# Kernel tuning notes

Measured on AMD Instinct MI355X. Metric: run time of the kernel, lower is better.

Reference implementation:

```python
import jax, jax.numpy as jnp
import numpy as np

B, C, H, W = 8, 128, 256, 256
N_POS, N_NEG = 2048, 8192
TEMPERATURE = 1.0
EPS = 1e-6


def setup_inputs() -> dict:
    key = jax.random.key(0)
    k0, k1, k2, k3, k4, k5, k6 = jax.random.split(key, 7)
    predict_seg_map = jax.random.normal(k0, (B, C, H, W), dtype=jnp.float32)
    # Random pixel-location samples (stand-in for nonzero+randperm sampling,
    # which the original detaches -> constants w.r.t. the loss).
    pos_b = jax.random.randint(k1, (N_POS,), 0, B, dtype=jnp.int32)
    pos_h = jax.random.randint(k2, (N_POS,), 0, H, dtype=jnp.int32)
    pos_w = jax.random.randint(k3, (N_POS,), 0, W, dtype=jnp.int32)
    neg_b = jax.random.randint(k4, (N_NEG,), 0, B, dtype=jnp.int32)
    neg_h = jax.random.randint(k5, (N_NEG,), 0, H, dtype=jnp.int32)
    neg_w = jax.random.randint(k6, (N_NEG,), 0, W, dtype=jnp.int32)
    return {
        "predict_seg_map": predict_seg_map,
        "pos_b": pos_b, "pos_h": pos_h, "pos_w": pos_w,
        "neg_b": neg_b, "neg_h": neg_h, "neg_w": neg_w,
    }


def _l2_normalize(x):
    # Matches nn.CosineSimilarity(dim=-1, eps=1e-6): clamp norm from below.
    n = jnp.sqrt(jnp.sum(x * x, axis=-1, keepdims=True))
    return x / jnp.maximum(n, EPS)


def reference(predict_seg_map, pos_b, pos_h, pos_w, neg_b, neg_h, neg_w):
    # Irregular gather of pixel embeddings: [N, C]
    pos_logits = predict_seg_map[pos_b, :, pos_h, pos_w]
    neg_logits = predict_seg_map[neg_b, :, neg_h, neg_w]

    pos_n = _l2_normalize(pos_logits)  # [N_POS, C]
    neg_n = _l2_normalize(neg_logits)  # [N_NEG, C]

    # Cosine similarity matrices via GEMM on unit vectors.
    pos_sim = jnp.einsum('ic,jc->ij', pos_n, pos_n)  # [N_POS, N_POS]
    neg_sim = jnp.einsum('ic,jc->ij', pos_n, neg_n)  # [N_POS, N_NEG]

    exp_pos = jnp.exp(pos_sim / TEMPERATURE)
    # Original subtracts exp(1.0) (diagonal self-similarity at T=1).
    pos_row_sum = jnp.sum(exp_pos, axis=1) - jnp.exp(jnp.float32(1.0))
    neg_row_sum = jnp.sum(jnp.exp(neg_sim / TEMPERATURE), axis=1)

    likelihood = pos_row_sum / (pos_row_sum + neg_row_sum)
    nll = -jnp.mean(jnp.log(likelihood))
    return nll
```

## Files before the change

kernel.cpp:

```cpp
#include <hip/hip_runtime.h>
#include <hip/hip_bf16.h>
#include <math.h>

#define BB      8
#define C_CH    128
#define HH      256
#define WW      256
#define N_POS   2048
#define N_NEG   8192
#define N_ROWS  (N_POS + N_NEG)
#define EPS_N   1e-6f

#define NI2     (N_POS / 64)
#define NJS     (N_ROWS / 64)
#define NJSLAB      (N_ROWS / 64)
#define NJSLAB_POS  (N_POS / 64)

#define PANEL   512

typedef __attribute__((ext_vector_type(8))) short bf16x8;
typedef __attribute__((ext_vector_type(4))) float f32x4;


__global__ __launch_bounds__(256) void gather_norm_kernel(
    const float* __restrict__ seg,
    const int* __restrict__ pb, const int* __restrict__ ph, const int* __restrict__ pw,
    const int* __restrict__ nb, const int* __restrict__ nh, const int* __restrict__ nw,
    ushort* __restrict__ hi_t, ushort* __restrict__ lo_t)
{
    const int wave = threadIdx.x >> 6;
    const int lane = threadIdx.x & 63;
    const int row  = blockIdx.x * 4 + wave;
    if (row >= N_ROWS) return;

    int b, h, w;
    if (row < N_POS) { b = pb[row]; h = ph[row]; w = pw[row]; }
    else { const int r = row - N_POS; b = nb[r]; h = nh[r]; w = nw[r]; }

    const size_t cs   = (size_t)HH * WW;
    const size_t base = (size_t)b * C_CH * cs + (size_t)h * WW + (size_t)w;

    const float v0 = seg[base + (size_t)lane * cs];
    const float v1 = seg[base + (size_t)(lane + 64) * cs];

    float ss = v0 * v0 + v1 * v1;
#pragma unroll
    for (int m = 1; m < 64; m <<= 1) ss += __shfl_xor(ss, m, 64);

    const float n  = fmaxf(sqrtf(ss), EPS_N);
    const float u0 = v0 / n;
    const float u1 = v1 / n;

    const __hip_bfloat16 h0 = __float2bfloat16(u0);
    const __hip_bfloat16 h1 = __float2bfloat16(u1);
    const __hip_bfloat16 l0 = __float2bfloat16(u0 - __bfloat162float(h0));
    const __hip_bfloat16 l1 = __float2bfloat16(u1 - __bfloat162float(h1));

    const int tile = row >> 4;
    const int lr   = row & 15;

    const int e0 = lane;
    const int ks0 = e0 >> 5, lk0 = (e0 & 31) >> 3, ke0 = e0 & 7;
    const size_t o0 = ((size_t)(tile * 4 + ks0) * 64 + lk0 * 16 + lr) * 8 + ke0;

    const int e1 = lane + 64;
    const int ks1 = e1 >> 5, lk1 = (e1 & 31) >> 3, ke1 = e1 & 7;
    const size_t o1 = ((size_t)(tile * 4 + ks1) * 64 + lk1 * 16 + lr) * 8 + ke1;

    hi_t[o0] = __hip_bfloat16_raw(h0).x;  lo_t[o0] = __hip_bfloat16_raw(l0).x;
    hi_t[o1] = __hip_bfloat16_raw(h1).x;  lo_t[o1] = __hip_bfloat16_raw(l1).x;
}

__global__ __launch_bounds__(64) void sim_mfma_kernel(
    const ushort* __restrict__ hi_t, const ushort* __restrict__ lo_t,
    float* __restrict__ partial)
{
    const int bid = blockIdx.x;
    const int it  = bid / NJS;
    const int js  = bid % NJS;
    const int lane = threadIdx.x & 63;

    const int iw0 = it * 64;

    const int lr = lane & 15;
    const int lk = lane >> 4;

    f32x4 acc[4][4];
#pragma unroll
    for (int m = 0; m < 4; ++m)
#pragma unroll
        for (int n = 0; n < 4; ++n) acc[m][n] = (f32x4){0.f, 0.f, 0.f, 0.f};

#pragma unroll
    for (int ks = 0; ks < 4; ++ks) {
        bf16x8 ah[4], al[4], bh[4], bl[4];
#pragma unroll
        for (int m = 0; m < 4; ++m) {
            const size_t pa = ((size_t)((it * 4 + m) * 4 + ks)) * PANEL + lane * 8;
            ah[m] = *(const bf16x8*)&hi_t[pa];
            al[m] = *(const bf16x8*)&lo_t[pa];
        }
#pragma unroll
        for (int n = 0; n < 4; ++n) {
            const size_t pb2 = ((size_t)((js * 4 + n) * 4 + ks)) * PANEL + lane * 8;
            bh[n] = *(const bf16x8*)&hi_t[pb2];
            bl[n] = *(const bf16x8*)&lo_t[pb2];
        }

#pragma unroll
        for (int n = 0; n < 4; ++n) {
#pragma unroll
            for (int m = 0; m < 4; ++m) {
                acc[m][n] = __builtin_amdgcn_mfma_f32_16x16x32_bf16(ah[m], bh[n], acc[m][n], 0, 0, 0);
                acc[m][n] = __builtin_amdgcn_mfma_f32_16x16x32_bf16(ah[m], bl[n], acc[m][n], 0, 0, 0);
                acc[m][n] = __builtin_amdgcn_mfma_f32_16x16x32_bf16(al[m], bh[n], acc[m][n], 0, 0, 0);
            }
        }
    }

#pragma unroll
    for (int m = 0; m < 4; ++m) {
        float s0 = 0.f, s1 = 0.f, s2 = 0.f, s3 = 0.f;
#pragma unroll
        for (int n = 0; n < 4; ++n) {
            s0 += expf(acc[m][n][0]);
            s1 += expf(acc[m][n][1]);
            s2 += expf(acc[m][n][2]);
            s3 += expf(acc[m][n][3]);
        }
        float s[4] = {s0, s1, s2, s3};
#pragma unroll
        for (int r = 0; r < 4; ++r) {
            float v = s[r];
            v += __shfl_xor(v, 1, 64);
            v += __shfl_xor(v, 2, 64);
            v += __shfl_xor(v, 4, 64);
            v += __shfl_xor(v, 8, 64);
            if (lr == 0) {
                const int row = iw0 + m * 16 + lk * 4 + r;
                partial[(size_t)js * N_POS + row] = v;
            }
        }
    }
}

__global__ __launch_bounds__(256) void rowred_kernel(
    const float* __restrict__ partial, float* __restrict__ bsum)
{
    const int t   = threadIdx.x;
    const int row = blockIdx.x * 256 + t;

    float P = 0.f;
#pragma unroll
    for (int s = 0; s < NJSLAB_POS; ++s) P += partial[(size_t)s * N_POS + row];

    float a0 = 0.f, a1 = 0.f, a2 = 0.f, a3 = 0.f;
    for (int s0 = NJSLAB_POS; s0 < NJSLAB; s0 += 16) {
        float v[16];
#pragma unroll
        for (int i = 0; i < 16; ++i)
            v[i] = partial[(size_t)(s0 + i) * N_POS + row];
#pragma unroll
        for (int i = 0; i < 16; i += 4) {
            a0 += v[i]; a1 += v[i + 1]; a2 += v[i + 2]; a3 += v[i + 3];
        }
    }
    const float Nv = (a0 + a1) + (a2 + a3);

    const float p = P - 2.71828182845904523536f;
    const float term = logf(p) - logf(p + Nv);

    __shared__ float red[256];
    red[t] = term;
    __syncthreads();
    for (int s = 128; s > 0; s >>= 1) {
        if (t < s) red[t] += red[t + s];
        __syncthreads();
    }
    if (t == 0) bsum[blockIdx.x] = red[0];
}

__global__ __launch_bounds__(64) void final_kernel(
    const float* __restrict__ bsum, float* __restrict__ out)
{
    if (threadIdx.x == 0) {
        float s = 0.f;
#pragma unroll
        for (int i = 0; i < N_POS / 256; ++i) s += bsum[i];
        out[0] = -s / (float)N_POS;
    }
}

extern "C" void kernel_launch(void* const* d_in, const int* in_sizes, int n_in,
                              void* d_out, int out_size, void* d_ws, size_t ws_size,
                              hipStream_t stream)
{
    const float* seg = (const float*)d_in[0];
    const int* pb = (const int*)d_in[1];
    const int* ph = (const int*)d_in[2];
    const int* pw = (const int*)d_in[3];
    const int* nb = (const int*)d_in[4];
    const int* nh = (const int*)d_in[5];
    const int* nw = (const int*)d_in[6];
    float* out = (float*)d_out;

    ushort* hi_t = (ushort*)d_ws;
    ushort* lo_t = hi_t + (size_t)N_ROWS * C_CH;
    float* partial = (float*)(lo_t + (size_t)N_ROWS * C_CH);
    float* bsum    = partial + (size_t)NJSLAB * N_POS;

    gather_norm_kernel<<<dim3((N_ROWS + 3) / 4), dim3(256), 0, stream>>>(
        seg, pb, ph, pw, nb, nh, nw, hi_t, lo_t);

    sim_mfma_kernel<<<dim3(NI2 * NJS), dim3(64), 0, stream>>>(hi_t, lo_t, partial);

    rowred_kernel<<<dim3(N_POS / 256), dim3(256), 0, stream>>>(partial, bsum);
    final_kernel<<<dim3(1), dim3(64), 0, stream>>>(bsum, out);
}
```

Measured before the change: 66.70 us.

## Share B slab across four waves via LDS in similarity MFMA kernel

Each block of the similarity kernel now runs four waves covering 256 query rows against one 64-row key slab. The key slab's hi/lo bf16 panels are staged once into shared memory and read by all four waves, instead of each single-wave block reloading them from global memory. This is meant to cut redundant global/L2 traffic for the B operand. The cost is 32 KB of LDS per block, which may limit occupancy, plus a block-wide barrier before compute.

```diff
diff --git a/kernel.cpp b/kernel.cpp
--- a/kernel.cpp
+++ b/kernel.cpp
@@ -11,7 +11,7 @@
 #define N_ROWS  (N_POS + N_NEG)
 #define EPS_N   1e-6f
 
-#define NI2     (N_POS / 64)
+#define NIG     (N_POS / 256)
 #define NJS     (N_ROWS / 64)
 #define NJSLAB      (N_ROWS / 64)
 #define NJSLAB_POS  (N_POS / 64)
@@ -71,19 +71,33 @@
     hi_t[o1] = __hip_bfloat16_raw(h1).x;  lo_t[o1] = __hip_bfloat16_raw(l1).x;
 }
 
-__global__ __launch_bounds__(64) void sim_mfma_kernel(
+__global__ __launch_bounds__(256) void sim_mfma_kernel(
     const ushort* __restrict__ hi_t, const ushort* __restrict__ lo_t,
     float* __restrict__ partial)
 {
+    __shared__ ushort ldsB[2][8192];
+
     const int bid = blockIdx.x;
-    const int it  = bid / NJS;
+    const int ig  = bid / NJS;
     const int js  = bid % NJS;
-    const int lane = threadIdx.x & 63;
-
-    const int iw0 = it * 64;
-
-    const int lr = lane & 15;
-    const int lk = lane >> 4;
+    const int t    = threadIdx.x;
+    const int wv   = t >> 6;
+    const int ln   = t & 63;
+
+    {
+        const size_t gb = (size_t)js * 8192;
+#pragma unroll
+        for (int c = 0; c < 4; ++c) {
+            const int off = (c * 256 + t) * 8;
+            *(bf16x8*)&ldsB[0][off] = *(const bf16x8*)&hi_t[gb + off];
+            *(bf16x8*)&ldsB[1][off] = *(const bf16x8*)&lo_t[gb + off];
+        }
+    }
+    __syncthreads();
+
+    const int iw0 = ig * 256 + wv * 64;
+    const int lr = ln & 15;
+    const int lk = ln >> 4;
 
     f32x4 acc[4][4];
 #pragma unroll
@@ -96,15 +110,15 @@
         bf16x8 ah[4], al[4], bh[4], bl[4];
 #pragma unroll
         for (int m = 0; m < 4; ++m) {
-            const size_t pa = ((size_t)((it * 4 + m) * 4 + ks)) * PANEL + lane * 8;
+            const size_t pa = ((size_t)((ig * 16 + wv * 4 + m) * 4 + ks)) * PANEL + ln * 8;
             ah[m] = *(const bf16x8*)&hi_t[pa];
             al[m] = *(const bf16x8*)&lo_t[pa];
         }
 #pragma unroll
         for (int n = 0; n < 4; ++n) {
-            const size_t pb2 = ((size_t)((js * 4 + n) * 4 + ks)) * PANEL + lane * 8;
-            bh[n] = *(const bf16x8*)&hi_t[pb2];
-            bl[n] = *(const bf16x8*)&lo_t[pb2];
+            const int lo_off = (n * 4 + ks) * PANEL + ln * 8;
+            bh[n] = *(const bf16x8*)&ldsB[0][lo_off];
+            bl[n] = *(const bf16x8*)&ldsB[1][lo_off];
         }
 
 #pragma unroll
@@ -212,7 +226,7 @@
     gather_norm_kernel<<<dim3((N_ROWS + 3) / 4), dim3(256), 0, stream>>>(
         seg, pb, ph, pw, nb, nh, nw, hi_t, lo_t);
 
-    sim_mfma_kernel<<<dim3(NI2 * NJS), dim3(64), 0, stream>>>(hi_t, lo_t, partial);
+    sim_mfma_kernel<<<dim3(NIG * NJS), dim3(256), 0, stream>>>(hi_t, lo_t, partial);
 
     rowred_kernel<<<dim3(N_POS / 256), dim3(256), 0, stream>>>(partial, bsum);
     final_kernel<<<dim3(1), dim3(64), 0, stream>>>(bsum, out);
```

Result: faster. 63.27 us (-5.1%).
